# Kernel tuning notes

Measured on AMD Instinct MI355X. Metric: run time of the kernel, lower is better.

Reference implementation:

```python
import jax, jax.numpy as jnp
import numpy as np

N, E, C, L, G, O = 100000, 1600000, 128, 7, 2, 40
BETA = 0.9
HEADS, HC = 1, 128  # heads=1, head_channels=hidden_channels=128


def setup_inputs() -> dict:
    key = jax.random.key(0)
    ks = jax.random.split(key, 16)
    s = 0.05  # ~ torch Linear init std for fan_in=128
    inp = {
        'x': jax.random.normal(ks[0], (N, C), jnp.float32),
        'edge_index': jax.random.randint(ks[1], (2, E), 0, N, jnp.int64),
        'Wh': jax.random.normal(ks[2], (L, C, C)) * s,
        'bh': jax.random.normal(ks[3], (L, C)) * s,
        'Wg': jax.random.normal(ks[4], (L, C, C)) * s,
        'bg': jax.random.normal(ks[5], (L, C)) * s,
        'Wl': jax.random.normal(ks[6], (L, C, C)) * s,
        'bl': jax.random.normal(ks[7], (L, C)) * s,
        'ln_g': jnp.ones((L, C)), 'ln_b': jnp.zeros((L, C)),
        'bn_g': jnp.ones((L, C)), 'bn_b': jnp.zeros((L, C)),
        'bn_rm': jnp.zeros((L, C)), 'bn_rv': jnp.ones((L, C)),
        'gWh': jax.random.normal(ks[8], (G, C, C)) * s,
        'gbh': jax.random.normal(ks[9], (G, C)) * s,
        'gWk': jax.random.normal(ks[10], (G, C, C)) * s,
        'gWv': jax.random.normal(ks[11], (G, C, C)) * s,
        'gln_g': jnp.ones((G, C)), 'gln_b': jnp.zeros((G, C)),
        'gWo': jax.random.normal(ks[12], (G, C, C)) * s,
        'gbo': jax.random.normal(ks[13], (G, C)) * s,
        'f_ln_g': jnp.ones((C,)), 'f_ln_b': jnp.zeros((C,)),
        'Wp': jax.random.normal(ks[14], (O, C)) * s,
        'bp': jax.random.normal(ks[15], (O,)) * s,
    }
    return inp


def _layer_norm(x, g, b, eps=1e-5):
    mu = jnp.mean(x, axis=-1, keepdims=True)
    var = jnp.mean((x - mu) ** 2, axis=-1, keepdims=True)
    return (x - mu) * jax.lax.rsqrt(var + eps) * g + b


def reference(x, edge_index, Wh, bh, Wg, bg, Wl, bl, ln_g, ln_b,
              bn_g, bn_b, bn_rm, bn_rv, gWh, gbh, gWk, gWv,
              gln_g, gln_b, gWo, gbo, f_ln_g, f_ln_b, Wp, bp):
    n = x.shape[0]
    src, dst = edge_index[0], edge_index[1]
    # gcn_norm with add_self_loops=True: deg over destination incl. self loop
    deg = jnp.zeros((n,), x.dtype).at[dst].add(1.0) + 1.0
    dinv = jax.lax.rsqrt(deg)
    enorm = (dinv[src] * dinv[dst])[:, None]   # [E,1]
    selfw = (dinv * dinv)[:, None]             # [N,1] self-loop weight

    x_local = jnp.zeros_like(x @ Wh[0].T)
    for i in range(L):
        h = jax.nn.relu(x @ Wh[i].T + bh[i])
        xw = x @ Wg[i].T                                  # GCN lin (bias separate)
        agg = jax.ops.segment_sum(xw[src] * enorm, dst, num_segments=n)
        conv = agg + xw * selfw + bg[i]
        x = conv + x @ Wl[i].T + bl[i]
        # BatchNorm1d in eval mode (running stats)
        x = (x - bn_rm[i]) * jax.lax.rsqrt(bn_rv[i] + 1e-5) * bn_g[i] + bn_b[i]
        x = jax.nn.relu(x)
        x = (1.0 - BETA) * _layer_norm(h * x, ln_g[i], ln_b[i]) + BETA * x
        x_local = x_local + x

    # global linear attention (PolynormerAttention, qk_shared=True, qkv_bias=False)
    xg = _layer_norm(x_local, f_ln_g, f_ln_b)
    for j in range(G):
        h = xg @ gWh[j].T + gbh[j]
        k = jax.nn.sigmoid(xg @ gWk[j].T).reshape(n, HEADS, HC)
        q = k
        v = (xg @ gWv[j].T).reshape(n, HEADS, HC)
        kv = jnp.einsum('ndh,ndm->dhm', k, v)            # [heads,hc,hc]
        num = jnp.einsum('ndh,dhm->ndm', q, kv)          # [N,heads,hc]
        k_sum = jnp.sum(k, axis=0)                       # [heads,hc]
        den = jnp.einsum('ndh,dh->nd', q, k_sum)[..., None]
        attn = (num / (den + 1e-6)).reshape(n, HEADS * HC)
        xg = _layer_norm(attn, gln_g[j], gln_b[j]) * (h + BETA)
        xg = jax.nn.relu(xg @ gWo[j].T + gbo[j])

    return xg @ Wp.T + bp
```

## Files before the change

### kernel.cpp

```cpp
#include <hip/hip_runtime.h>

typedef unsigned short u16;
typedef unsigned int u32;
typedef __attribute__((ext_vector_type(8))) short short8;
typedef __attribute__((ext_vector_type(8))) unsigned short ushort8v;
typedef __attribute__((ext_vector_type(4))) float f32x4;

#define CDIM 128

__device__ __forceinline__ float b2f(u16 u){ return __uint_as_float(((unsigned)u)<<16); }
__device__ __forceinline__ u16 f2b(float f){
  unsigned x = __float_as_uint(f);
  unsigned r = (x + 0x7fffu + ((x>>16)&1u)) >> 16;
  return (u16)r;
}
__device__ __forceinline__ float wsum64(float v){
  #pragma unroll
  for(int d=1; d<64; d<<=1) v += __shfl_xor(v, d, 64);
  return v;
}
__device__ __forceinline__ float wsum16(float v){
  v += __shfl_xor(v, 1, 64);
  v += __shfl_xor(v, 2, 64);
  v += __shfl_xor(v, 4, 64);
  v += __shfl_xor(v, 8, 64);
  return v;
}

__global__ void k_probe(const u32* __restrict__ x, const u32* __restrict__ ei, int* __restrict__ flags){
  __shared__ int s_bf, s_nz;
  if(threadIdx.x == 0){ s_bf = 0; s_nz = 0; }
  __syncthreads();
  int c_bf = 0, c_nz = 0;
  for(int i = threadIdx.x; i < 4096; i += 256){
    u32 w = x[i];
    u32 e = (w >> 7) & 0xFFu;
    if(e >= 100u && e <= 140u) c_bf++;
    if(ei[2*i + 1] != 0u) c_nz++;
  }
  atomicAdd(&s_bf, c_bf);
  atomicAdd(&s_nz, c_nz);
  __syncthreads();
  if(threadIdx.x == 0){
    flags[0] = (s_bf < 2048) ? 1 : 0;
    flags[1] = (s_nz < 8) ? 1 : 0;
  }
}

__global__ void k_cvt_x(const void* __restrict__ src, u16* __restrict__ dst, int n,
                        const int* __restrict__ flags){
  int i = (blockIdx.x*256 + threadIdx.x)*8;
  if(i + 7 >= n) return;
  if(flags[0]){
    const float* s = (const float*)src + i;
    float4 a = *(const float4*)s;
    float4 b = *(const float4*)(s + 4);
    ushort8v o;
    o[0]=f2b(a.x); o[1]=f2b(a.y); o[2]=f2b(a.z); o[3]=f2b(a.w);
    o[4]=f2b(b.x); o[5]=f2b(b.y); o[6]=f2b(b.z); o[7]=f2b(b.w);
    *(ushort8v*)(dst + i) = o;
  } else {
    *(ushort8v*)(dst + i) = *(const ushort8v*)((const u16*)src + i);
  }
}

struct CvtArgs {
  const void* src[24];
  u16* dst[24];
  int n[24];
};

__global__ void k_cvt_params(CvtArgs a, const int* __restrict__ flags){
  int seg = blockIdx.y;
  int i = blockIdx.x*256 + threadIdx.x;
  int n = a.n[seg];
  if(i >= n) return;
  if(flags[0]) a.dst[seg][i] = f2b(((const float*)a.src[seg])[i]);
  else         a.dst[seg][i] = ((const u16*)a.src[seg])[i];
}

__global__ void k_cvt_ei_count(const int* __restrict__ src, int* __restrict__ dst, int E,
                               const int* __restrict__ flags, u32* __restrict__ cnt){
  int i = blockIdx.x*256 + threadIdx.x;
  if(i >= 2*E) return;
  int v = flags[1] ? src[2*i] : src[i];
  dst[i] = v;
  if(i >= E) atomicAdd(&cnt[v], 1u);
}

__global__ __launch_bounds__(256) void k_scan1(const u32* __restrict__ cnt, int n, u32* __restrict__ bsum){
  const int lane = threadIdx.x & 63;
  const int wv = threadIdx.x >> 6;
  int i = blockIdx.x*256 + threadIdx.x;
  u32 v = (i < n) ? cnt[i] : 0u;
  #pragma unroll
  for(int d=1; d<64; d<<=1) v += (u32)__shfl_xor((int)v, d, 64);
  __shared__ u32 ws[4];
  if(lane == 0) ws[wv] = v;
  __syncthreads();
  if(threadIdx.x == 0) bsum[blockIdx.x] = ws[0] + ws[1] + ws[2] + ws[3];
}

__global__ __launch_bounds__(1024) void k_scan2(const u32* __restrict__ bsum, int nb, u32* __restrict__ bpre){
  __shared__ u32 s[1024];
  int t = threadIdx.x;
  u32 v = (t < nb) ? bsum[t] : 0u;
  s[t] = v;
  __syncthreads();
  for(int d=1; d<1024; d<<=1){
    u32 y = (t >= d) ? s[t-d] : 0u;
    __syncthreads();
    s[t] += y;
    __syncthreads();
  }
  if(t < nb) bpre[t] = s[t] - v;
}

__global__ __launch_bounds__(256) void k_scan3(const u32* __restrict__ cnt, int n,
                                               const u32* __restrict__ bpre,
                                               u32* __restrict__ rowstart, u32* __restrict__ cursor,
                                               float* __restrict__ dinv){
  const int lane = threadIdx.x & 63;
  const int wv = threadIdx.x >> 6;
  int i = blockIdx.x*256 + threadIdx.x;
  u32 v = (i < n) ? cnt[i] : 0u;
  u32 x = v;
  #pragma unroll
  for(int d=1; d<64; d<<=1){
    u32 y = (u32)__shfl_up((int)x, d, 64);
    if(lane >= d) x += y;
  }
  __shared__ u32 ws[4];
  if(lane == 63) ws[wv] = x;
  __syncthreads();
  u32 woff = 0;
  #pragma unroll
  for(int w=0; w<4; w++) if(w < wv) woff += ws[w];
  u32 incl = x + woff;
  u32 rs = bpre[blockIdx.x] + incl - v;
  if(i < n){
    rowstart[i] = rs;
    cursor[i] = rs;
    dinv[i] = rsqrtf((float)(v + 1u));
    if(i == n-1) rowstart[n] = rs + v;
  }
}

__global__ __launch_bounds__(256) void k_scatter8(
  const int* __restrict__ ei, int E, int Nn, int nsl,
  u32* __restrict__ cursor, const float* __restrict__ dinv, int2* __restrict__ colw)
{
  const int r = blockIdx.x & 7;
  const int slice = blockIdx.x >> 3;
  const int q = (Nn + 7) >> 3;
  const int lo = r*q;
  const int hi = (lo + q < Nn) ? lo + q : Nn;
  const int chunk = (E + nsl - 1) / nsl;
  int e0 = slice*chunk;
  int e1 = e0 + chunk; if(e1 > E) e1 = E;
  for(int e = e0 + threadIdx.x; e < e1; e += 256){
    int d = ei[E + e];
    if(d >= lo && d < hi){
      int s = ei[e];
      u32 p = atomicAdd(&cursor[d], 1u);
      colw[p] = make_int2(s, __float_as_int(dinv[s]));
    }
  }
}

__global__ __launch_bounds__(256) void k_gemm3(
  const u16* __restrict__ A, int M,
  const u16* __restrict__ W0, const u16* __restrict__ bs0, int op0, u16* __restrict__ O0,
  const u16* __restrict__ W1, const u16* __restrict__ bs1, int op1, u16* __restrict__ O1,
  const u16* __restrict__ W2, const u16* __restrict__ bs2, int op2, u16* __restrict__ O2)
{
  const int lane = threadIdx.x & 63;
  const int wv = threadIdx.x >> 6;
  const int l16 = lane & 15, quad = lane >> 4;
  const long nbase = (long)blockIdx.x*256 + wv*64;

  const u16* Ws[3] = {W0, W1, W2};
  const u16* Bs[3] = {bs0, bs1, bs2};
  u16* Os[3] = {O0, O1, O2};
  const int ops[3] = {op0, op1, op2};
  const int w = blockIdx.y;
  const u16* Wm = Ws[w];
  const int op = ops[w];
  u16* Op = Os[w];
  const u16* bp = Bs[w];

  short8 xf[4][4];
  #pragma unroll
  for(int nt=0; nt<4; nt++){
    long r = nbase + nt*16 + l16; if(r >= M) r = M-1;
    const u16* ap = A + r*CDIM + quad*8;
    #pragma unroll
    for(int kt=0; kt<4; kt++)
      xf[nt][kt] = *(const short8*)(ap + kt*32);
  }

  #pragma unroll
  for(int ct=0; ct<8; ct++){
    f32x4 acc[4];
    #pragma unroll
    for(int nt=0; nt<4; nt++) acc[nt] = (f32x4){0.f,0.f,0.f,0.f};
    const u16* wp = Wm + (ct*16 + l16)*CDIM + quad*8;
    #pragma unroll
    for(int kt=0; kt<4; kt++){
      short8 wf = *(const short8*)(wp + kt*32);
      #pragma unroll
      for(int nt=0; nt<4; nt++)
        acc[nt] = __builtin_amdgcn_mfma_f32_16x16x32_bf16(wf, xf[nt][kt], acc[nt], 0, 0, 0);
    }
    float bv[4] = {0.f,0.f,0.f,0.f};
    if(bp){
      ushort4 bq = *(const ushort4*)(bp + ct*16 + quad*4);
      bv[0]=b2f(bq.x); bv[1]=b2f(bq.y); bv[2]=b2f(bq.z); bv[3]=b2f(bq.w);
    }
    #pragma unroll
    for(int nt=0; nt<4; nt++){
      long node = nbase + nt*16 + l16;
      if(node < M){
        u16 o[4];
        #pragma unroll
        for(int g=0; g<4; g++){
          float v = acc[nt][g] + bv[g];
          if(op == 1) v = fmaxf(v, 0.f);
          else if(op == 2) v = 1.f/(1.f + __expf(-v));
          o[g] = f2b(v);
        }
        u32 p0 = (u32)o[0] | ((u32)o[1] << 16);
        u32 p1 = (u32)o[2] | ((u32)o[3] << 16);
        *(uint2*)(Op + (size_t)node*CDIM + ct*16 + quad*4) = make_uint2(p0, p1);
      }
    }
  }
}

__global__ __launch_bounds__(256) void k_layer_epi(
  const u16* __restrict__ xw, const u16* __restrict__ h, const u16* __restrict__ xl,
  const int2* __restrict__ colw, const u32* __restrict__ rowstart, const float* __restrict__ dinv,
  const u16* __restrict__ bg, const u16* __restrict__ bng, const u16* __restrict__ bnb,
  const u16* __restrict__ bnrm, const u16* __restrict__ bnrv,
  const u16* __restrict__ lng, const u16* __restrict__ lnb,
  const u16* __restrict__ flng, const u16* __restrict__ flnb,
  float* __restrict__ xlocal, u16* __restrict__ xout, int n, int first, int final)
{
  const int lane = threadIdx.x & 63;
  const int quad = lane >> 4;
  const int l16 = lane & 15;
  const int wv = threadIdx.x >> 6;
  int node = blockIdx.x*16 + wv*4 + quad;
  const int valid = (node < n);
  if(!valid) node = n - 1;
  const int cg = l16*8;
  u32 j0 = rowstart[node], j1 = rowstart[node+1];
  float a[8];
  #pragma unroll
  for(int g=0; g<8; g++) a[g] = 0.f;

  for(u32 base = j0; base < j1; base += 16){
    int cnt = (int)(j1 - base); if(cnt > 16) cnt = 16;
    int2 pw = make_int2(0, 0);
    if(l16 < cnt) pw = colw[base + l16];
    ushort8v v[16]; float w[16];
    #pragma unroll
    for(int u=0; u<16; u++){
      int s = __shfl(pw.x, quad*16 + u, 64);
      w[u] = __int_as_float(__shfl(pw.y, quad*16 + u, 64));
      v[u] = *(const ushort8v*)(xw + (size_t)s*CDIM + cg);
    }
    #pragma unroll
    for(int u=0; u<16; u++){
      #pragma unroll
      for(int g=0; g<8; g++) a[g] = fmaf(w[u], b2f(v[u][g]), a[g]);
    }
  }

  float dn = dinv[node], sw = dn*dn;
  size_t nb = (size_t)node*CDIM + cg;
  ushort8v xwv  = *(const ushort8v*)(xw + nb);
  ushort8v xlv  = *(const ushort8v*)(xl + nb);
  ushort8v hv   = *(const ushort8v*)(h  + nb);
  ushort8v bgv  = *(const ushort8v*)(bg + cg);
  ushort8v bngv = *(const ushort8v*)(bng + cg);
  ushort8v bnbv = *(const ushort8v*)(bnb + cg);
  ushort8v bnrmv= *(const ushort8v*)(bnrm + cg);
  ushort8v bnrvv= *(const ushort8v*)(bnrv + cg);
  ushort8v lngv = *(const ushort8v*)(lng + cg);
  ushort8v lnbv = *(const ushort8v*)(lnb + cg);

  float x3[8], t[8];
  float ts = 0.f;
  #pragma unroll
  for(int g=0; g<8; g++){
    float x1 = a[g]*dn + b2f(xwv[g])*sw + b2f(bgv[g]) + b2f(xlv[g]);
    float sc = rsqrtf(b2f(bnrvv[g]) + 1e-5f) * b2f(bngv[g]);
    float x2 = (x1 - b2f(bnrmv[g]))*sc + b2f(bnbv[g]);
    x3[g] = fmaxf(x2, 0.f);
    t[g] = b2f(hv[g]) * x3[g];
    ts += t[g];
  }
  float mu = wsum16(ts) * (1.f/128.f);
  float vs = 0.f;
  #pragma unroll
  for(int g=0; g<8; g++){ float d = t[g] - mu; vs = fmaf(d, d, vs); }
  float inv = rsqrtf(wsum16(vs)*(1.f/128.f) + 1e-5f);

  float xn[8], xl2[8];
  #pragma unroll
  for(int g=0; g<8; g++){
    float y = (t[g] - mu)*inv*b2f(lngv[g]) + b2f(lnbv[g]);
    xn[g] = 0.1f*y + 0.9f*x3[g];
  }
  if(first){
    #pragma unroll
    for(int g=0; g<8; g++) xl2[g] = xn[g];
  } else {
    f32x4 p0 = *(const f32x4*)(xlocal + nb);
    f32x4 p1 = *(const f32x4*)(xlocal + nb + 4);
    xl2[0]=p0[0]+xn[0]; xl2[1]=p0[1]+xn[1]; xl2[2]=p0[2]+xn[2]; xl2[3]=p0[3]+xn[3];
    xl2[4]=p1[0]+xn[4]; xl2[5]=p1[1]+xn[5]; xl2[6]=p1[2]+xn[6]; xl2[7]=p1[3]+xn[7];
  }
  if(!final){
    if(valid){
      f32x4 q0 = {xl2[0],xl2[1],xl2[2],xl2[3]};
      f32x4 q1 = {xl2[4],xl2[5],xl2[6],xl2[7]};
      *(f32x4*)(xlocal + nb)     = q0;
      *(f32x4*)(xlocal + nb + 4) = q1;
      ushort8v o;
      #pragma unroll
      for(int g=0; g<8; g++) o[g] = f2b(xn[g]);
      *(ushort8v*)(xout + nb) = o;
    }
  } else {
    float ss = 0.f;
    #pragma unroll
    for(int g=0; g<8; g++) ss += xl2[g];
    float mu2 = wsum16(ss) * (1.f/128.f);
    float v2 = 0.f;
    #pragma unroll
    for(int g=0; g<8; g++){ float e = xl2[g] - mu2; v2 = fmaf(e, e, v2); }
    float inv2 = rsqrtf(wsum16(v2)*(1.f/128.f) + 1e-5f);
    ushort8v flngv = *(const ushort8v*)(flng + cg);
    ushort8v flnbv = *(const ushort8v*)(flnb + cg);
    if(valid){
      ushort8v o;
      #pragma unroll
      for(int g=0; g<8; g++)
        o[g] = f2b((xl2[g] - mu2)*inv2*b2f(flngv[g]) + b2f(flnbv[g]));
      *(ushort8v*)(xout + nb) = o;
    }
  }
}

__global__ __launch_bounds__(256) void k_kv(
  const u16* __restrict__ kk, const u16* __restrict__ vv, int n, int npb,
  float* __restrict__ part)
{
  __shared__ float sk[8][128];
  __shared__ float sv[8][128];
  const int tid = threadIdx.x;
  const int tr = tid >> 4, tc = tid & 15;
  float acc[8][8];
  #pragma unroll
  for(int i=0;i<8;i++){
    #pragma unroll
    for(int j=0;j<8;j++) acc[i][j] = 0.f;
  }
  float ks[8];
  #pragma unroll
  for(int i=0;i<8;i++) ks[i] = 0.f;
  int start = blockIdx.x * npb;
  int end = start + npb; if(end > n) end = n;
  const int lr = tid >> 5;
  const int lc = (tid & 31) * 4;
  for(int g0 = start; g0 < end; g0 += 8){
    int cnt = end - g0; if(cnt > 8) cnt = 8;
    __syncthreads();
    if(lr < cnt){
      ushort4 kq = *(const ushort4*)(kk + (size_t)(g0+lr)*CDIM + lc);
      ushort4 vq = *(const ushort4*)(vv + (size_t)(g0+lr)*CDIM + lc);
      sk[lr][lc] = b2f(kq.x); sk[lr][lc+1] = b2f(kq.y); sk[lr][lc+2] = b2f(kq.z); sk[lr][lc+3] = b2f(kq.w);
      sv[lr][lc] = b2f(vq.x); sv[lr][lc+1] = b2f(vq.y); sv[lr][lc+2] = b2f(vq.z); sv[lr][lc+3] = b2f(vq.w);
    }
    __syncthreads();
    for(int r=0; r<cnt; r++){
      float4 ka = *(const float4*)&sk[r][tr*8];
      float4 kb = *(const float4*)&sk[r][tr*8+4];
      float4 va = *(const float4*)&sv[r][tc*8];
      float4 vb = *(const float4*)&sv[r][tc*8+4];
      float kr[8] = {ka.x,ka.y,ka.z,ka.w,kb.x,kb.y,kb.z,kb.w};
      float vr[8] = {va.x,va.y,va.z,va.w,vb.x,vb.y,vb.z,vb.w};
      #pragma unroll
      for(int i=0;i<8;i++){
        #pragma unroll
        for(int j=0;j<8;j++) acc[i][j] = fmaf(kr[i], vr[j], acc[i][j]);
      }
      if(tc == 0){
        #pragma unroll
        for(int i=0;i<8;i++) ks[i] += kr[i];
      }
    }
  }
  float* p = part + (size_t)blockIdx.x * 16512;
  #pragma unroll
  for(int i=0;i<8;i++){
    #pragma unroll
    for(int j=0;j<8;j++)
      p[(size_t)(tc*8+j)*CDIM + tr*8 + i] = acc[i][j];
  }
  if(tc == 0){
    #pragma unroll
    for(int i=0;i<8;i++) p[16384 + tr*8 + i] = ks[i];
  }
}

__global__ void k_kvred(const float* __restrict__ part, int nb, u16* __restrict__ Bext){
  int i = blockIdx.x*256 + threadIdx.x;
  if(i >= 144*128) return;
  float s = 0.f;
  if(i < 16512){
    #pragma unroll 8
    for(int b=0;b<nb;b++) s += part[(size_t)b*16512 + i];
  }
  Bext[i] = f2b(s);
}

__global__ __launch_bounds__(256) void k_attn(
  const u16* __restrict__ q, const u16* __restrict__ Bext, const u16* __restrict__ hg,
  const u16* __restrict__ g, const u16* __restrict__ b,
  const u16* __restrict__ Wo, const u16* __restrict__ bo,
  const u16* __restrict__ Wp, const u16* __restrict__ bp,
  u16* __restrict__ xgout, void* __restrict__ outv,
  int M, int last, const int* __restrict__ flags)
{
  __shared__ u16 stg[4][32*136];
  const int lane = threadIdx.x & 63;
  const int wv = threadIdx.x >> 6;
  const int l16 = lane & 15, quad = lane >> 4;
  const long rbase = (long)blockIdx.x*128 + wv*32;
  u16* st = stg[wv];

  {
    short8 af[2][4];
    #pragma unroll
    for(int rt=0; rt<2; rt++){
      long r = rbase + rt*16 + l16; if(r >= M) r = M-1;
      const u16* ap = q + r*CDIM + quad*8;
      #pragma unroll
      for(int kt=0; kt<4; kt++)
        af[rt][kt] = *(const short8*)(ap + kt*32);
    }
    f32x4 acc[2][9];
    f32x4 zero = {0.f,0.f,0.f,0.f};
    #pragma unroll
    for(int rt=0; rt<2; rt++){
      #pragma unroll
      for(int ct=0; ct<9; ct++) acc[rt][ct] = zero;
    }
    #pragma unroll
    for(int ct=0; ct<9; ct++){
      const u16* wp = Bext + (ct*16 + l16)*CDIM + quad*8;
      #pragma unroll
      for(int kt=0; kt<4; kt++){
        short8 bf = *(const short8*)(wp + kt*32);
        acc[0][ct] = __builtin_amdgcn_mfma_f32_16x16x32_bf16(af[0][kt], bf, acc[0][ct], 0, 0, 0);
        acc[1][ct] = __builtin_amdgcn_mfma_f32_16x16x32_bf16(af[1][kt], bf, acc[1][ct], 0, 0, 0);
      }
    }
    #pragma unroll
    for(int rt=0; rt<2; rt++){
      float rden[4];
      #pragma unroll
      for(int gi=0; gi<4; gi++){
        float dv = __shfl(acc[rt][8][gi], lane & 48, 64);
        rden[gi] = 1.f/(dv + 1e-6f);
      }
      #pragma unroll
      for(int gi=0; gi<4; gi++){
        float sum = 0.f;
        #pragma unroll
        for(int ct=0; ct<8; ct++) sum += acc[rt][ct][gi]*rden[gi];
        float mu = wsum16(sum) * (1.f/128.f);
        float vs = 0.f;
        #pragma unroll
        for(int ct=0; ct<8; ct++){ float d = acc[rt][ct][gi]*rden[gi] - mu; vs = fmaf(d, d, vs); }
        float inv = rsqrtf(wsum16(vs)*(1.f/128.f) + 1e-5f);
        const int rowl = rt*16 + quad*4 + gi;
        #pragma unroll
        for(int ct=0; ct<8; ct++){
          int col = ct*16 + l16;
          float y = (acc[rt][ct][gi]*rden[gi] - mu)*inv*b2f(g[col]) + b2f(b[col]);
          st[rowl*136 + col] = f2b(y);
        }
      }
    }
  }
  #pragma unroll
  for(int p2=0; p2<8; p2++){
    int row = (p2>>2)*16 + (lane>>2);
    int seg = (lane&3) + (p2&3)*4;
    long node = rbase + row;
    if(node >= M) node = M-1;
    ushort8v yv = *(const ushort8v*)&st[row*136 + seg*8];
    ushort8v hv = *(const ushort8v*)(hg + (size_t)node*CDIM + seg*8);
    ushort8v o;
    #pragma unroll
    for(int i2=0; i2<8; i2++)
      o[i2] = f2b(b2f(yv[i2]) * (b2f(hv[i2]) + 0.9f));
    *(ushort8v*)&st[row*136 + seg*8] = o;
  }
  short8 pf[2][4];
  #pragma unroll
  for(int nt=0; nt<2; nt++){
    #pragma unroll
    for(int kt=0; kt<4; kt++)
      pf[nt][kt] = *(const short8*)&st[(nt*16 + l16)*136 + quad*8 + kt*32];
  }
  #pragma unroll
  for(int ct=0; ct<8; ct++){
    f32x4 a0 = {0.f,0.f,0.f,0.f}, a1 = {0.f,0.f,0.f,0.f};
    const u16* wp = Wo + (ct*16 + l16)*CDIM + quad*8;
    #pragma unroll
    for(int kt=0; kt<4; kt++){
      short8 wf = *(const short8*)(wp + kt*32);
      a0 = __builtin_amdgcn_mfma_f32_16x16x32_bf16(wf, pf[0][kt], a0, 0, 0, 0);
      a1 = __builtin_amdgcn_mfma_f32_16x16x32_bf16(wf, pf[1][kt], a1, 0, 0, 0);
    }
    ushort4 bq = *(const ushort4*)(bo + ct*16 + quad*4);
    float bv[4] = {b2f(bq.x), b2f(bq.y), b2f(bq.z), b2f(bq.w)};
    #pragma unroll
    for(int nt=0; nt<2; nt++){
      f32x4 a = nt ? a1 : a0;
      u16 o[4];
      #pragma unroll
      for(int g2=0; g2<4; g2++)
        o[g2] = f2b(fmaxf(a[g2] + bv[g2], 0.f));
      u32 p0 = (u32)o[0] | ((u32)o[1] << 16);
      u32 p1 = (u32)o[2] | ((u32)o[3] << 16);
      *(uint2*)&st[(nt*16 + l16)*136 + ct*16 + quad*4] = make_uint2(p0, p1);
    }
  }
  if(!last){
    #pragma unroll
    for(int p2=0; p2<8; p2++){
      int row = (p2>>2)*16 + (lane>>2);
      int seg = (lane&3) + (p2&3)*4;
      long node = rbase + row;
      ushort8v v = *(const ushort8v*)&st[row*136 + seg*8];
      if(node < M)
        *(ushort8v*)(xgout + (size_t)node*CDIM + seg*8) = v;
    }
  } else {
    const int f32m = flags[0];
    short8 pf2[2][4];
    #pragma unroll
    for(int nt=0; nt<2; nt++){
      #pragma unroll
      for(int kt=0; kt<4; kt++)
        pf2[nt][kt] = *(const short8*)&st[(nt*16 + l16)*136 + quad*8 + kt*32];
    }
    #pragma unroll
    for(int ct=0; ct<3; ct++){
      f32x4 a0 = {0.f,0.f,0.f,0.f}, a1 = {0.f,0.f,0.f,0.f};
      int wrow = ct*16 + l16; if(wrow > 39) wrow = 39;
      const u16* wp = Wp + wrow*CDIM + quad*8;
      #pragma unroll
      for(int kt=0; kt<4; kt++){
        short8 wf = *(const short8*)(wp + kt*32);
        a0 = __builtin_amdgcn_mfma_f32_16x16x32_bf16(wf, pf2[0][kt], a0, 0, 0, 0);
        a1 = __builtin_amdgcn_mfma_f32_16x16x32_bf16(wf, pf2[1][kt], a1, 0, 0, 0);
      }
      const int ch0 = ct*16 + quad*4;
      if(ch0 < 40){
        ushort4 bq = *(const ushort4*)(bp + ch0);
        float bv[4] = {b2f(bq.x), b2f(bq.y), b2f(bq.z), b2f(bq.w)};
        #pragma unroll
        for(int nt=0; nt<2; nt++){
          long node = rbase + nt*16 + l16;
          if(node < M){
            f32x4 a = nt ? a1 : a0;
            if(f32m){
              float* op = (float*)outv + node*40 + ch0;
              #pragma unroll
              for(int g2=0; g2<4; g2++) op[g2] = a[g2] + bv[g2];
            } else {
              u16 o[4];
              #pragma unroll
              for(int g2=0; g2<4; g2++) o[g2] = f2b(a[g2] + bv[g2]);
              u32 p0 = (u32)o[0] | ((u32)o[1] << 16);
              u32 p1 = (u32)o[2] | ((u32)o[3] << 16);
              *(uint2*)((u16*)outv + node*40 + ch0) = make_uint2(p0, p1);
            }
          }
        }
      }
    }
  }
}

extern "C" void kernel_launch(void* const* d_in, const int* in_sizes, int n_in,
                              void* d_out, int out_size, void* d_ws, size_t ws_size,
                              hipStream_t stream)
{
  (void)n_in;
  const int C = CDIM;
  const int Nn = in_sizes[0] / C;
  const int E  = in_sizes[1] / 2;

  char* ws = (char*)d_ws;
  size_t off = 0;
  auto alloc = [&](size_t bytes) -> char* {
    char* p = ws + off;
    off = (off + bytes + 255) & ~(size_t)255;
    return p;
  };
  u16*   x_cur  = (u16*)  alloc((size_t)Nn*C*2);
  float* xlocal = (float*)alloc((size_t)Nn*C*4);
  u16*   hb     = (u16*)  alloc((size_t)Nn*C*2);
  u16*   xwb    = (u16*)  alloc((size_t)Nn*C*2);
  u16*   xlb    = (u16*)  alloc((size_t)Nn*C*2);
  float* dinv   = (float*)alloc((size_t)Nn*4);
  u32*   cnt    = (u32*)  alloc((size_t)Nn*4);
  u32*   rowst  = (u32*)  alloc((size_t)(Nn+1)*4);
  u32*   cursor = (u32*)  alloc((size_t)Nn*4);
  int2*  colw   = (int2*) alloc((size_t)E*8);
  u16*   Bext   = (u16*)  alloc((size_t)144*128*2);
  int*   flags  = (int*)  alloc(256);
  u32*   bsum   = (u32*)  alloc(1024*4);
  u32*   bpre   = (u32*)  alloc(1024*4);
  size_t ptot = 0;
  for(int k=2;k<26;k++) ptot += (size_t)in_sizes[k];
  u16* pbuf = (u16*)alloc(ptot*2);

  if(off > ws_size){
    hipMemsetAsync(d_out, 0, (size_t)out_size*2, stream);
    return;
  }

  const u16* pp[26];
  {
    size_t po = 0;
    for(int k=2;k<26;k++){ pp[k] = pbuf + po; po += (size_t)in_sizes[k]; }
  }
  const u16* cWh  = pp[2];  const u16* cbh  = pp[3];
  const u16* cWg  = pp[4];  const u16* cbg  = pp[5];
  const u16* cWl  = pp[6];  const u16* cbl  = pp[7];
  const u16* clng = pp[8];  const u16* clnb = pp[9];
  const u16* cbng = pp[10]; const u16* cbnb = pp[11];
  const u16* cbnrm= pp[12]; const u16* cbnrv= pp[13];
  const u16* cgWh = pp[14]; const u16* cgbh = pp[15];
  const u16* cgWk = pp[16]; const u16* cgWv = pp[17];
  const u16* cglng= pp[18]; const u16* cglnb= pp[19];
  const u16* cgWo = pp[20]; const u16* cgbo = pp[21];
  const u16* cflng= pp[22]; const u16* cflnb= pp[23];
  const u16* cWp  = pp[24]; const u16* cbp  = pp[25];

  u16* xb  = (u16*)xlocal;
  int* eib = (int*)((char*)xlocal + (size_t)Nn*C*2);
  u16* xg  = x_cur;
  float* kvpart = xlocal;

  const int NB_KV = 512;
  const int npb = (Nn + NB_KV - 1) / NB_KV;
  const int gblk = (Nn + 127) / 128;
  const int gblk2 = (Nn + 255) / 256;
  const int nodeblk = (Nn + 15) / 16;
  const int nscan = (Nn + 255) / 256;
  const int NSL = 512;

  k_probe<<<1, 256, 0, stream>>>((const u32*)d_in[0], (const u32*)d_in[1], flags);
  hipMemsetAsync(cnt, 0, (size_t)Nn*4, stream);
  k_cvt_ei_count<<<(2*E + 255)/256, 256, 0, stream>>>((const int*)d_in[1], eib, E, flags, cnt);
  k_cvt_x<<<(Nn*C/8 + 255)/256, 256, 0, stream>>>(d_in[0], xb, Nn*C, flags);
  {
    CvtArgs a;
    int maxn = 0;
    for(int k=2;k<26;k++){
      a.src[k-2] = d_in[k];
      a.dst[k-2] = (u16*)pp[k];
      a.n[k-2]   = in_sizes[k];
      if(in_sizes[k] > maxn) maxn = in_sizes[k];
    }
    dim3 g((maxn + 255)/256, 24);
    k_cvt_params<<<g, 256, 0, stream>>>(a, flags);
  }

  k_scan1<<<nscan, 256, 0, stream>>>(cnt, Nn, bsum);
  k_scan2<<<1, 1024, 0, stream>>>(bsum, nscan, bpre);
  k_scan3<<<nscan, 256, 0, stream>>>(cnt, Nn, bpre, rowst, cursor, dinv);
  k_scatter8<<<NSL*8, 256, 0, stream>>>(eib, E, Nn, NSL, cursor, dinv, colw);

  const u16* xa = xb;
  for(int i=0; i<7; i++){
    k_gemm3<<<dim3(gblk2,3), 256, 0, stream>>>(xa, Nn,
        cWh + (size_t)i*C*C, cbh + (size_t)i*C, 1, hb,
        cWg + (size_t)i*C*C, (const u16*)nullptr, 0, xwb,
        cWl + (size_t)i*C*C, cbl + (size_t)i*C, 0, xlb);
    k_layer_epi<<<nodeblk, 256, 0, stream>>>(xwb, hb, xlb, colw, rowst, dinv,
        cbg + (size_t)i*C, cbng + (size_t)i*C, cbnb + (size_t)i*C,
        cbnrm + (size_t)i*C, cbnrv + (size_t)i*C,
        clng + (size_t)i*C, clnb + (size_t)i*C,
        cflng, cflnb,
        xlocal, x_cur, Nn, (i==0) ? 1 : 0, (i==6) ? 1 : 0);
    xa = x_cur;
  }

  for(int j=0; j<2; j++){
    k_gemm3<<<dim3(gblk2,3), 256, 0, stream>>>(xg, Nn,
        cgWh + (size_t)j*C*C, cgbh + (size_t)j*C, 0, hb,
        cgWk + (size_t)j*C*C, (const u16*)nullptr, 2, xwb,
        cgWv + (size_t)j*C*C, (const u16*)nullptr, 0, xlb);
    k_kv   <<<NB_KV, 256, 0, stream>>>(xwb, xlb, Nn, npb, kvpart);
    k_kvred<<<(144*128 + 255)/256, 256, 0, stream>>>(kvpart, NB_KV, Bext);
    k_attn <<<gblk, 256, 0, stream>>>(xwb, Bext, hb,
        cglng + (size_t)j*C, cglnb + (size_t)j*C,
        cgWo + (size_t)j*C*C, cgbo + (size_t)j*C,
        cWp, cbp, xg, d_out, Nn, (j==1) ? 1 : 0, flags);
  }
}
```

Measured before the change: 1.668 ms.

## Fuse three GEMMs per block and stage outputs through LDS for coalesced stores

The triple GEMM kernel now has each block handle 128 nodes and loop over all three weight matrices, instead of launching one grid dimension per matrix with 256 nodes per block. The A-tile is then loaded once for all three outputs, which cuts repeated reads of the activation matrix. Results go to a per-wave shared-memory staging buffer and are written as full 16-byte row chunks, replacing scattered 8-byte stores. The cost is fewer MFMA tiles per wave (2 instead of 4) for each weight fragment load, plus extra LDS traffic.

Result: no change. 1.689 ms (+1.3%).

```diff
diff --git a/kernel.cpp b/kernel.cpp
--- a/kernel.cpp
+++ b/kernel.cpp
@@ -174,24 +174,16 @@
   const u16* __restrict__ W1, const u16* __restrict__ bs1, int op1, u16* __restrict__ O1,
   const u16* __restrict__ W2, const u16* __restrict__ bs2, int op2, u16* __restrict__ O2)
 {
+  __shared__ u16 stg[4][32][72];
   const int lane = threadIdx.x & 63;
   const int wv = threadIdx.x >> 6;
   const int l16 = lane & 15, quad = lane >> 4;
-  const long nbase = (long)blockIdx.x*256 + wv*64;
-
-  const u16* Ws[3] = {W0, W1, W2};
-  const u16* Bs[3] = {bs0, bs1, bs2};
-  u16* Os[3] = {O0, O1, O2};
-  const int ops[3] = {op0, op1, op2};
-  const int w = blockIdx.y;
-  const u16* Wm = Ws[w];
-  const int op = ops[w];
-  u16* Op = Os[w];
-  const u16* bp = Bs[w];
-
-  short8 xf[4][4];
-  #pragma unroll
-  for(int nt=0; nt<4; nt++){
+  const long nbase = (long)blockIdx.x*128 + wv*32;
+  u16 (*st)[72] = stg[wv];
+
+  short8 xf[2][4];
+  #pragma unroll
+  for(int nt=0; nt<2; nt++){
     long r = nbase + nt*16 + l16; if(r >= M) r = M-1;
     const u16* ap = A + r*CDIM + quad*8;
     #pragma unroll
@@ -199,39 +191,56 @@
       xf[nt][kt] = *(const short8*)(ap + kt*32);
   }
 
-  #pragma unroll
-  for(int ct=0; ct<8; ct++){
-    f32x4 acc[4];
-    #pragma unroll
-    for(int nt=0; nt<4; nt++) acc[nt] = (f32x4){0.f,0.f,0.f,0.f};
-    const u16* wp = Wm + (ct*16 + l16)*CDIM + quad*8;
-    #pragma unroll
-    for(int kt=0; kt<4; kt++){
-      short8 wf = *(const short8*)(wp + kt*32);
-      #pragma unroll
-      for(int nt=0; nt<4; nt++)
-        acc[nt] = __builtin_amdgcn_mfma_f32_16x16x32_bf16(wf, xf[nt][kt], acc[nt], 0, 0, 0);
-    }
-    float bv[4] = {0.f,0.f,0.f,0.f};
-    if(bp){
-      ushort4 bq = *(const ushort4*)(bp + ct*16 + quad*4);
-      bv[0]=b2f(bq.x); bv[1]=b2f(bq.y); bv[2]=b2f(bq.z); bv[3]=b2f(bq.w);
-    }
-    #pragma unroll
-    for(int nt=0; nt<4; nt++){
-      long node = nbase + nt*16 + l16;
-      if(node < M){
-        u16 o[4];
+  const int srow = lane >> 3;
+  const int schk = lane & 7;
+
+  #pragma unroll
+  for(int w=0; w<3; w++){
+    const u16* Wm = (w==0) ? W0 : (w==1) ? W1 : W2;
+    const u16* bp = (w==0) ? bs0 : (w==1) ? bs1 : bs2;
+    const int  op = (w==0) ? op0 : (w==1) ? op1 : op2;
+    u16*       Op = (w==0) ? O0 : (w==1) ? O1 : O2;
+    #pragma unroll
+    for(int half=0; half<2; half++){
+      #pragma unroll
+      for(int c2=0; c2<4; c2++){
+        const int ct = half*4 + c2;
+        f32x4 acc0 = {0.f,0.f,0.f,0.f}, acc1 = {0.f,0.f,0.f,0.f};
+        const u16* wp = Wm + (ct*16 + l16)*CDIM + quad*8;
         #pragma unroll
-        for(int g=0; g<4; g++){
-          float v = acc[nt][g] + bv[g];
-          if(op == 1) v = fmaxf(v, 0.f);
-          else if(op == 2) v = 1.f/(1.f + __expf(-v));
-          o[g] = f2b(v);
+        for(int kt=0; kt<4; kt++){
+          short8 wf = *(const short8*)(wp + kt*32);
+          acc0 = __builtin_amdgcn_mfma_f32_16x16x32_bf16(wf, xf[0][kt], acc0, 0, 0, 0);
+          acc1 = __builtin_amdgcn_mfma_f32_16x16x32_bf16(wf, xf[1][kt], acc1, 0, 0, 0);
         }
-        u32 p0 = (u32)o[0] | ((u32)o[1] << 16);
-        u32 p1 = (u32)o[2] | ((u32)o[3] << 16);
-        *(uint2*)(Op + (size_t)node*CDIM + ct*16 + quad*4) = make_uint2(p0, p1);
+        float bv[4] = {0.f,0.f,0.f,0.f};
+        if(bp){
+          ushort4 bq = *(const ushort4*)(bp + ct*16 + quad*4);
+          bv[0]=b2f(bq.x); bv[1]=b2f(bq.y); bv[2]=b2f(bq.z); bv[3]=b2f(bq.w);
+        }
+        #pragma unroll
+        for(int nt=0; nt<2; nt++){
+          f32x4 a = nt ? acc1 : acc0;
+          u16 o[4];
+          #pragma unroll
+          for(int g=0; g<4; g++){
+            float v = a[g] + bv[g];
+            if(op == 1) v = fmaxf(v, 0.f);
+            else if(op == 2) v = 1.f/(1.f + __expf(-v));
+            o[g] = f2b(v);
+          }
+          u32 p0 = (u32)o[0] | ((u32)o[1] << 16);
+          u32 p1 = (u32)o[2] | ((u32)o[3] << 16);
+          *(uint2*)&st[nt*16 + l16][c2*16 + quad*4] = make_uint2(p0, p1);
+        }
+      }
+      #pragma unroll
+      for(int i=0; i<4; i++){
+        int row = i*8 + srow;
+        long node = nbase + row;
+        ushort8v v = *(const ushort8v*)&st[row][schk*8];
+        if(node < M)
+          *(ushort8v*)(Op + (size_t)node*CDIM + half*64 + schk*8) = v;
       }
     }
   }
@@ -665,7 +674,6 @@
   const int NB_KV = 512;
   const int npb = (Nn + NB_KV - 1) / NB_KV;
   const int gblk = (Nn + 127) / 128;
-  const int gblk2 = (Nn + 255) / 256;
   const int nodeblk = (Nn + 15) / 16;
   const int nscan = (Nn + 255) / 256;
   const int NSL = 512;
@@ -694,7 +702,7 @@
 
   const u16* xa = xb;
   for(int i=0; i<7; i++){
-    k_gemm3<<<dim3(gblk2,3), 256, 0, stream>>>(xa, Nn,
+    k_gemm3<<<gblk, 256, 0, stream>>>(xa, Nn,
         cWh + (size_t)i*C*C, cbh + (size_t)i*C, 1, hb,
         cWg + (size_t)i*C*C, (const u16*)nullptr, 0, xwb,
         cWl + (size_t)i*C*C, cbl + (size_t)i*C, 0, xlb);
@@ -708,7 +716,7 @@
   }
 
   for(int j=0; j<2; j++){
-    k_gemm3<<<dim3(gblk2,3), 256, 0, stream>>>(xg, Nn,
+    k_gemm3<<<gblk, 256, 0, stream>>>(xg, Nn,
         cgWh + (size_t)j*C*C, cgbh + (size_t)j*C, 0, hb,
         cgWk + (size_t)j*C*C, (const u16*)nullptr, 2, xwb,
         cgWv + (size_t)j*C*C, (const u16*)nullptr, 0, xlb);
```
